# Performance work log

Measured on AMD Instinct MI355X. Metric: run time of the kernel, lower is better.

## Reference

```python
import jax, jax.numpy as jnp
import numpy as np
from jax import lax

B, S, H, E, P, K, R = 64, 512, 768, 32, 16, 9, 6
HEADS, C1, C2 = 4, 128, 64
FEAT = 4 * C2 + 1  # e1, e2, e1*e2, context (64 each) + log-distance


def _ln(x, g, b):
    m = x.mean(-1, keepdims=True)
    v = ((x - m) ** 2).mean(-1, keepdims=True)
    return (x - m) * lax.rsqrt(v + 1e-5) * g + b


def _gat(x, adj, W, a_s, a_d, bias, heads, cout, concat):
    # Dense GATConv over a small fully-masked entity graph. adj[b,i,j]=edge j->i (incl. self-loops).
    h = jnp.einsum('bef,fhc->behc', x, W.reshape(x.shape[-1], heads, cout))
    s = jnp.einsum('behc,hc->bhe', h, a_s)  # source-node attention term
    d = jnp.einsum('behc,hc->bhe', h, a_d)  # target-node attention term
    logits = jax.nn.leaky_relu(d[:, :, :, None] + s[:, :, None, :], 0.2)  # [b,h,i,j]
    logits = jnp.where(adj[:, None, :, :], logits, -1e9)
    att = jax.nn.softmax(logits, axis=-1)
    out = jnp.einsum('bhij,bjhc->bihc', att, h)
    out = out.reshape(out.shape[0], out.shape[1], heads * cout) if concat else out.mean(2)
    return out + bias


def _crf_nll(em, tags, mask, start, end, trans):
    # torchcrf: loss = -mean log-likelihood. em [B,S,K]; tags [B,S]; mask [B,S] bool.
    emt = jnp.transpose(em, (1, 0, 2))
    tgt = tags.T
    mkt = mask.T.astype(em.dtype)
    num0 = start[tgt[0]] + jnp.take_along_axis(emt[0], tgt[0][:, None], 1)[:, 0]

    def nstep(c, inp):
        ptag, sc = c
        e, t, m = inp
        step = trans[ptag, t] + jnp.take_along_axis(e, t[:, None], 1)[:, 0]
        return (jnp.where(m > 0, t, ptag), sc + step * m), None

    (ltag, num), _ = lax.scan(nstep, (tgt[0], num0), (emt[1:], tgt[1:], mkt[1:]))
    num = num + end[ltag]
    a0 = start[None, :] + emt[0]

    def dstep(a, inp):
        e, m = inp
        nxt = jax.scipy.special.logsumexp(a[:, :, None] + trans[None] + e[:, None, :], axis=1)
        return jnp.where(m[:, None] > 0, nxt, a), None

    aT, _ = lax.scan(dstep, a0, (emt[1:], mkt[1:]))
    Z = jax.scipy.special.logsumexp(aT + end[None], axis=1)
    return jnp.mean(Z - num)


def setup_inputs() -> dict:
    key = jax.random.key(0)
    ks = jax.random.split(key, 24)
    n = lambda i, shape, s=0.05: jax.random.normal(ks[i], shape, jnp.float32) * s
    return {
        'sequence_output': jax.random.normal(ks[0], (B, S, H), jnp.float32),
        'attention_mask': jnp.ones((B, S), jnp.int32),
        'ner_labels': jax.random.randint(ks[1], (B, S), 0, K),
        'entity_start': jax.random.randint(ks[2], (B, E), 0, S - 8),
        'entity_len': jax.random.randint(ks[3], (B, E), 0, 8),
        'pair_e1': jax.random.randint(ks[4], (B, P), 0, E),
        'pair_e2': jax.random.randint(ks[5], (B, P), 0, E),
        'pair_labels': jax.random.randint(ks[6], (B, P), 0, 2),
        'adj_mask': jnp.ones((B, E, E), bool),
        'w_ner1': n(7, (H, 256)), 'b_ner1': jnp.zeros((256,), jnp.float32),
        'w_ner2': n(8, (256, K)), 'b_ner2': jnp.zeros((K,), jnp.float32),
        'crf_start': n(9, (K,), 0.1), 'crf_end': n(10, (K,), 0.1), 'crf_trans': n(11, (K, K), 0.1),
        'w_gat1': n(12, (H, HEADS * C1)), 'a_src1': n(13, (HEADS, C1)), 'a_dst1': n(14, (HEADS, C1)),
        'b_gat1': jnp.zeros((HEADS * C1,), jnp.float32),
        'w_gat2': n(15, (HEADS * C1, C2)), 'a_src2': n(16, (1, C2)), 'a_dst2': n(17, (1, C2)),
        'b_gat2': jnp.zeros((C2,), jnp.float32),
        'w_fe': n(18, (FEAT, 512)), 'b_fe': jnp.zeros((512,), jnp.float32),
        'g_fe': jnp.ones((512,), jnp.float32), 'be_fe': jnp.zeros((512,), jnp.float32),
        'w_rc1': n(19, (R, 512, 256)), 'b_rc1': jnp.zeros((R, 256), jnp.float32),
        'g_rc': jnp.ones((R, 256), jnp.float32), 'be_rc': jnp.zeros((R, 256), jnp.float32),
        'w_rc2': n(20, (R, 256, 1)), 'b_rc2': jnp.zeros((R,), jnp.float32),
    }


def reference(sequence_output, attention_mask, ner_labels, entity_start, entity_len,
              pair_e1, pair_e2, pair_labels, adj_mask,
              w_ner1, b_ner1, w_ner2, b_ner2, crf_start, crf_end, crf_trans,
              w_gat1, a_src1, a_dst1, b_gat1, w_gat2, a_src2, a_dst2, b_gat2,
              w_fe, b_fe, g_fe, be_fe, w_rc1, b_rc1, g_rc, be_rc, w_rc2, b_rc2):
    # NER head (dropout off / eval)
    ner_logits = jnp.maximum(sequence_output @ w_ner1 + b_ner1, 0.0) @ w_ner2 + b_ner2
    ner_loss = _crf_nll(ner_logits, ner_labels, attention_mask.astype(bool),
                        crf_start, crf_end, crf_trans)
    # entity span mean-pool via inclusive cumsum trick
    cs = jnp.concatenate([jnp.zeros((B, 1, H), sequence_output.dtype),
                          jnp.cumsum(sequence_output, axis=1)], axis=1)
    e_end = jnp.clip(entity_start + entity_len, 0, S - 1)
    seg = (jnp.take_along_axis(cs, (e_end + 1)[:, :, None], 1)
           - jnp.take_along_axis(cs, entity_start[:, :, None], 1))
    ent = seg / (e_end - entity_start + 1).astype(sequence_output.dtype)[:, :, None]  # [B,E,H]
    x = _gat(ent, adj_mask, w_gat1, a_src1, a_dst1, b_gat1, HEADS, C1, True)
    x = jnp.maximum(x, 0.0)
    x = _gat(x, adj_mask, w_gat2, a_src2, a_dst2, b_gat2, 1, C2, False)  # [B,E,64]
    x1 = jnp.take_along_axis(x, pair_e1[:, :, None], 1)
    x2 = jnp.take_along_axis(x, pair_e2[:, :, None], 1)
    ctx = jnp.broadcast_to(x.mean(1, keepdims=True), (B, P, C2))
    dist = jnp.log(jnp.abs(pair_e1 - pair_e2).astype(x.dtype) + 1.0)[:, :, None]
    pf = jnp.concatenate([x1, x2, x1 * x2, ctx, dist], axis=-1)  # [B,P,257]
    fe = jax.nn.leaky_relu(_ln(pf @ w_fe + b_fe, g_fe, be_fe), 0.01)
    h1 = jnp.einsum('bpf,rfo->rbpo', fe, w_rc1) + b_rc1[:, None, None, :]
    h1 = jax.nn.leaky_relu(_ln(h1, g_rc[:, None, None, :], be_rc[:, None, None, :]), 0.01)
    z = jnp.einsum('rbpo,ro->rbp', h1, w_rc2[:, :, 0]) + b_rc2[:, None, None]
    y = pair_labels.astype(z.dtype)[None]
    # BCEWithLogitsLoss(pos_weight=2.0), mean per relation type, summed over types
    bce = -(2.0 * y * jax.nn.log_sigmoid(z) + (1.0 - y) * jax.nn.log_sigmoid(-z))
    rel_loss = bce.mean(axis=(1, 2)).sum()
    total = ner_loss + rel_loss
    return ner_logits, z, total
```

## Files before the change

kernel.cpp:

```cpp
#include <hip/hip_runtime.h>
#include <math.h>


#define NB 64
#define NS 512
#define NH 768
#define NE 32
#define NP 16
#define NK 9
#define NR 6
#define NHEADS 4
#define NC1 128
#define NC2 64
#define SEGS 16
#define SEGLEN 32

#define ZOFF 294912
#define TOTOFF 301056

#define WS_ENT   0u
#define WS_HG1   1572864u
#define WS_X1    2621440u
#define WS_H2    3670016u
#define WS_X2    3801088u
#define WS_S1    3932160u
#define WS_D1    3940352u
#define WS_S2    3948544u
#define WS_D2    3950592u
#define WS_CTX   3952640u
#define WS_PF    3956736u
#define WS_FE    4222976u
#define WS_CRF   4747264u
#define WS_REL   4747328u
#define WS_W1T   4747392u
#define WS_WRT   0u
#define WS_WFET  393216u
#define WS_SEG   475136u

typedef __attribute__((ext_vector_type(8))) short bf16x8;
typedef __attribute__((ext_vector_type(4))) float f32x4;

__device__ __forceinline__ unsigned short f2bf(float x) {
  union { float f; unsigned u; } v; v.f = x;
  unsigned r = v.u + 0x7FFFu + ((v.u >> 16) & 1u);
  return (unsigned short)(r >> 16);
}

__device__ __forceinline__ float logsigf(float x) {
  if (x >= 0.f) return -log1pf(__expf(-x));
  return x - log1pf(__expf(x));
}

__global__ __launch_bounds__(256) void k_w1t(const float* __restrict__ w1,
    unsigned short* __restrict__ w1t) {
  const int k = blockIdx.x, t = threadIdx.x;
  w1t[t * NH + k] = f2bf(w1[k * 256 + t]);
}

__global__ __launch_bounds__(256) void k_wrt(const float* __restrict__ w1,
    unsigned short* __restrict__ wrt) {
  __shared__ unsigned short tr[256 * 72];
  const int r = blockIdx.x >> 3, kt = blockIdx.x & 7;
  const int k0 = kt * 64, t = threadIdx.x;
#pragma unroll
  for (int i = 0; i < 16; i++) {
    const int slot = t + 256 * i;
    const int row = slot >> 6, c4 = slot & 63;
    const float4 f = *reinterpret_cast<const float4*>(
        &w1[((size_t)(r * 512) + k0 + row) * 256 + c4 * 4]);
    tr[(c4 * 4 + 0) * 72 + row] = f2bf(f.x);
    tr[(c4 * 4 + 1) * 72 + row] = f2bf(f.y);
    tr[(c4 * 4 + 2) * 72 + row] = f2bf(f.z);
    tr[(c4 * 4 + 3) * 72 + row] = f2bf(f.w);
  }
  __syncthreads();
#pragma unroll
  for (int i = 0; i < 8; i++) {
    const int slot = t + 256 * i;
    const int col = slot >> 3, q = slot & 7;
    *reinterpret_cast<uint4*>(&wrt[((size_t)(r * 256 + col)) * 512 + k0 + q * 8]) =
        *reinterpret_cast<const uint4*>(&tr[col * 72 + q * 8]);
  }
}

__global__ __launch_bounds__(256) void k_wfet(const float* __restrict__ w,
    unsigned short* __restrict__ wt) {
  __shared__ unsigned short tr[256 * 72];
  const int kt = blockIdx.x % 5, cb = blockIdx.x / 5;
  const int k0 = kt * 64, c0 = cb * 256, t = threadIdx.x;
#pragma unroll
  for (int i = 0; i < 16; i++) {
    const int slot = t + 256 * i;
    const int row = slot >> 6, c4 = slot & 63;
    const int k = k0 + row;
    float4 f = {0.f, 0.f, 0.f, 0.f};
    if (k < 257)
      f = *reinterpret_cast<const float4*>(&w[(size_t)k * 512 + c0 + c4 * 4]);
    tr[(c4 * 4 + 0) * 72 + row] = f2bf(f.x);
    tr[(c4 * 4 + 1) * 72 + row] = f2bf(f.y);
    tr[(c4 * 4 + 2) * 72 + row] = f2bf(f.z);
    tr[(c4 * 4 + 3) * 72 + row] = f2bf(f.w);
  }
  __syncthreads();
#pragma unroll
  for (int i = 0; i < 8; i++) {
    const int slot = t + 256 * i;
    const int col = slot >> 3, q = slot & 7;
    *reinterpret_cast<uint4*>(&wt[((size_t)(c0 + col)) * 320 + k0 + q * 8]) =
        *reinterpret_cast<const uint4*>(&tr[col * 72 + q * 8]);
  }
}

__global__ __launch_bounds__(256) void k_ner(const float* __restrict__ seq,
    const unsigned short* __restrict__ w1t, const float* __restrict__ b1,
    const float* __restrict__ w2, const float* __restrict__ b2,
    float* __restrict__ out) {
  __shared__ unsigned short AsS[64 * 40];
  __shared__ unsigned short BsS[256 * 40];
  __shared__ float zs[64 * 4 * 12];
  const int t = threadIdx.x;
  const int tok0 = blockIdx.x * 64;
  const int w = t >> 6, lane = t & 63, quad = lane >> 4, l15 = lane & 15;

  f32x4 acc[4][4];
#pragma unroll
  for (int r = 0; r < 4; r++)
#pragma unroll
    for (int c = 0; c < 4; c++) acc[r][c] = (f32x4){0.f, 0.f, 0.f, 0.f};

  const int tokA = t >> 2, koffA = (t & 3) * 8;
  const float* aptr = seq + (size_t)(tok0 + tokA) * NH + koffA;

  for (int kt = 0; kt < NH; kt += 32) {
    __syncthreads();
    {
      const float4 f0 = *reinterpret_cast<const float4*>(aptr + kt);
      const float4 f1 = *reinterpret_cast<const float4*>(aptr + kt + 4);
      bf16x8 av;
      av[0] = (short)f2bf(f0.x); av[1] = (short)f2bf(f0.y);
      av[2] = (short)f2bf(f0.z); av[3] = (short)f2bf(f0.w);
      av[4] = (short)f2bf(f1.x); av[5] = (short)f2bf(f1.y);
      av[6] = (short)f2bf(f1.z); av[7] = (short)f2bf(f1.w);
      *reinterpret_cast<bf16x8*>(&AsS[tokA * 40 + koffA]) = av;
    }
#pragma unroll
    for (int i = 0; i < 4; i++) {
      const int q = t + 256 * i;
      const int col = q >> 2, koff = (q & 3) * 8;
      *reinterpret_cast<uint4*>(&BsS[col * 40 + koff]) =
          *reinterpret_cast<const uint4*>(&w1t[(size_t)col * NH + kt + koff]);
    }
    __syncthreads();
    bf16x8 a[4], b[4];
#pragma unroll
    for (int r = 0; r < 4; r++)
      a[r] = *reinterpret_cast<const bf16x8*>(&AsS[(r * 16 + l15) * 40 + quad * 8]);
#pragma unroll
    for (int c = 0; c < 4; c++)
      b[c] = *reinterpret_cast<const bf16x8*>(&BsS[(w * 64 + c * 16 + l15) * 40 + quad * 8]);
#pragma unroll
    for (int r = 0; r < 4; r++)
#pragma unroll
      for (int c = 0; c < 4; c++)
        acc[r][c] = __builtin_amdgcn_mfma_f32_16x16x32_bf16(a[r], b[c], acc[r][c], 0, 0, 0);
  }

  float b1v[4], w2v[4][NK];
#pragma unroll
  for (int c = 0; c < 4; c++) {
    const int col = w * 64 + c * 16 + l15;
    b1v[c] = b1[col];
#pragma unroll
    for (int cc = 0; cc < NK; cc++) w2v[c][cc] = w2[col * NK + cc];
  }
#pragma unroll
  for (int r = 0; r < 4; r++) {
#pragma unroll
    for (int reg = 0; reg < 4; reg++) {
      float p[NK];
#pragma unroll
      for (int cc = 0; cc < NK; cc++) p[cc] = 0.f;
#pragma unroll
      for (int c = 0; c < 4; c++) {
        const float h = fmaxf(acc[r][c][reg] + b1v[c], 0.f);
#pragma unroll
        for (int cc = 0; cc < NK; cc++) p[cc] = fmaf(h, w2v[c][cc], p[cc]);
      }
#pragma unroll
      for (int o = 1; o < 16; o <<= 1)
#pragma unroll
        for (int cc = 0; cc < NK; cc++) p[cc] += __shfl_xor(p[cc], o);
      if (l15 == 0) {
        const int tokr = r * 16 + quad * 4 + reg;
#pragma unroll
        for (int cc = 0; cc < NK; cc++) zs[(tokr * 4 + w) * 12 + cc] = p[cc];
      }
    }
  }
  __syncthreads();
  if (t < 64) {
#pragma unroll
    for (int cc = 0; cc < NK; cc++) {
      const float z = zs[(t * 4 + 0) * 12 + cc] + zs[(t * 4 + 1) * 12 + cc] +
                      zs[(t * 4 + 2) * 12 + cc] + zs[(t * 4 + 3) * 12 + cc] + b2[cc];
      out[(size_t)(tok0 + t) * NK + cc] = z;
    }
  }
}

__global__ __launch_bounds__(128) void k_crf_seg(const float* __restrict__ em,
    const int* __restrict__ mask, const float* __restrict__ trans,
    float* __restrict__ segm) {
  __shared__ float bufA[16 * 81];
  __shared__ float bufB[8 * 81];
  __shared__ float ems[SEGLEN * 9];
  __shared__ int mks[SEGLEN];
  __shared__ float trs[81];
  const int blk = blockIdx.x;
  const int b = blk >> 4, seg = blk & 15;
  const int t = threadIdx.x;
  const int s0 = 1 + seg * SEGLEN;
  const float* emb = em + (size_t)b * NS * NK;
  const int* mk = mask + b * NS;
  if (t < 81) trs[t] = trans[t];
  for (int i = t; i < SEGLEN * 9; i += 128) {
    const int g = s0 * 9 + i;
    ems[i] = (g < NS * 9) ? emb[g] : 0.f;
  }
  if (t < SEGLEN) {
    const int s = s0 + t;
    mks[t] = (s < NS) ? mk[s] : 0;
  }
  __syncthreads();
  for (int idx = t; idx < 16 * 81; idx += 128) {
    const int p = idx / 81, e = idx % 81, i = e / 9, j = e % 9;
    const int la = 2 * p, lb = la + 1;
    const bool ma = mks[la] > 0, mb = mks[lb] > 0;
    float r;
    if (ma && mb) {
      float v[9], mx = -1e30f;
#pragma unroll
      for (int m = 0; m < 9; m++) {
        v[m] = trs[i * 9 + m] + ems[la * 9 + m] + trs[m * 9 + j];
        mx = fmaxf(mx, v[m]);
      }
      float sum = 0.f;
#pragma unroll
      for (int m = 0; m < 9; m++) sum += __expf(v[m] - mx);
      r = mx + __logf(sum) + ems[lb * 9 + j];
    } else if (ma) {
      r = trs[e] + ems[la * 9 + j];
    } else if (mb) {
      r = trs[e] + ems[lb * 9 + j];
    } else {
      r = (i == j) ? 0.f : -1e30f;
    }
    bufA[p * 81 + e] = r;
  }
  float* src = bufA;
  float* dst = bufB;
  for (int n = 16; n > 1; n >>= 1) {
    __syncthreads();
    const int half = n >> 1;
    for (int idx = t; idx < half * 81; idx += 128) {
      const int q = idx / 81, e = idx % 81, i = e / 9, j = e % 9;
      const float* A = src + (size_t)(2 * q) * 81;
      const float* Bm = src + (size_t)(2 * q + 1) * 81;
      float v[9], mx = -1e30f;
#pragma unroll
      for (int m = 0; m < 9; m++) {
        v[m] = A[i * 9 + m] + Bm[m * 9 + j];
        mx = fmaxf(mx, v[m]);
      }
      float sum = 0.f;
#pragma unroll
      for (int m = 0; m < 9; m++) sum += __expf(v[m] - mx);
      dst[q * 81 + e] = mx + __logf(sum);
    }
    float* tmp = src; src = dst; dst = tmp;
  }
  __syncthreads();
  if (t < 81) segm[((size_t)b * SEGS + seg) * 81 + t] = src[t];
}

__global__ __launch_bounds__(64) void k_crf_fin(const float* __restrict__ em,
    const int* __restrict__ tags, const int* __restrict__ mask,
    const float* __restrict__ startv, const float* __restrict__ endv,
    const float* __restrict__ trans, const float* __restrict__ segm,
    float* __restrict__ lossb) {
  __shared__ float sm[SEGS * 81];
  __shared__ float av[16];
  __shared__ float red[2];
  const int b = blockIdx.x, t = threadIdx.x;
  const float* emb = em + (size_t)b * NS * NK;
  const int* mk = mask + b * NS;
  const int* tg = tags + b * NS;
  for (int i = t; i < SEGS * 81; i += 64) sm[i] = segm[(size_t)b * SEGS * 81 + i];
  {
    float num = 0.f;
    int lastS = 0;
#pragma unroll
    for (int o = 0; o < 8; o++) {
      const int s = t * 8 + o;
      if (s >= 1 && mk[s] > 0) {
        const int cur = tg[s], prv = tg[s - 1];
        num += trans[prv * NK + cur] + emb[s * NK + cur];
        lastS = s;
      }
    }
#pragma unroll
    for (int o = 32; o > 0; o >>= 1) {
      num += __shfl_xor(num, o);
      lastS = max(lastS, __shfl_xor(lastS, o));
    }
    if (t == 0) {
      const int t0 = tg[0];
      red[0] = startv[t0] + emb[t0] + num + endv[tg[lastS]];
    }
  }
  __syncthreads();
  if (t < 9) av[t] = startv[t] + emb[t];
  __syncthreads();
  for (int h = 0; h < SEGS; h++) {
    float nv = 0.f;
    if (t < 9) {
      float v[9], mx = -1e30f;
#pragma unroll
      for (int i2 = 0; i2 < 9; i2++) {
        v[i2] = av[i2] + sm[h * 81 + i2 * 9 + t];
        mx = fmaxf(mx, v[i2]);
      }
      float sum = 0.f;
#pragma unroll
      for (int i2 = 0; i2 < 9; i2++) sum += __expf(v[i2] - mx);
      nv = mx + __logf(sum);
    }
    __syncthreads();
    if (t < 9) av[t] = nv;
    __syncthreads();
  }
  if (t == 0) {
    float mx = -1e30f;
#pragma unroll
    for (int j = 0; j < 9; j++) mx = fmaxf(mx, av[j] + endv[j]);
    float sum = 0.f;
#pragma unroll
    for (int j = 0; j < 9; j++) sum += __expf(av[j] + endv[j] - mx);
    lossb[b] = (mx + __logf(sum)) - red[0];
  }
}

__global__ __launch_bounds__(256) void k_ent(const float* __restrict__ seq,
    const int* __restrict__ est, const int* __restrict__ elen, float* __restrict__ ent) {
  const int be = blockIdx.x;
  const int b = be >> 5, e = be & 31;
  const int st = est[b * NE + e];
  int en = st + elen[b * NE + e];
  en = min(max(en, 0), NS - 1);
  const float inv = 1.f / (float)(en - st + 1);
  for (int c = threadIdx.x; c < NH; c += 256) {
    float s = 0.f;
    for (int r = st; r <= en; r++) s += seq[((size_t)b * NS + r) * NH + c];
    ent[((size_t)b * NE + e) * NH + c] = s * inv;
  }
}

__global__ __launch_bounds__(256) void k_g1(const float* __restrict__ ent,
    const float* __restrict__ w, float* __restrict__ hout) {
  __shared__ float As[32 * 36];
  __shared__ float Bs[32 * 128];
  const int b = blockIdx.x >> 2, cb = blockIdx.x & 3;
  const int t = threadIdx.x;
  const int tc = t & 31, tr = t >> 5;
  float acc[4][4];
#pragma unroll
  for (int i = 0; i < 4; i++)
#pragma unroll
    for (int j = 0; j < 4; j++) acc[i][j] = 0.f;
  for (int kt = 0; kt < NH; kt += 32) {
    __syncthreads();
    {
      const int e = t >> 3, k4 = t & 7;
      *reinterpret_cast<float4*>(&As[e * 36 + k4 * 4]) =
          *reinterpret_cast<const float4*>(&ent[((size_t)b * NE + e) * NH + kt + k4 * 4]);
    }
#pragma unroll
    for (int i = 0; i < 4; i++) {
      const int slot = t + 256 * i;
      const int row = slot >> 5, cg = slot & 31;
      *reinterpret_cast<float4*>(&Bs[row * 128 + cg * 4]) =
          *reinterpret_cast<const float4*>(&w[(size_t)(kt + row) * 512 + cb * 128 + cg * 4]);
    }
    __syncthreads();
#pragma unroll
    for (int kg = 0; kg < 8; kg++) {
      float4 a[4];
#pragma unroll
      for (int i = 0; i < 4; i++)
        a[i] = *reinterpret_cast<const float4*>(&As[(tr * 4 + i) * 36 + kg * 4]);
#pragma unroll
      for (int k2 = 0; k2 < 4; k2++) {
        const float4 bv = *reinterpret_cast<const float4*>(&Bs[(kg * 4 + k2) * 128 + tc * 4]);
#pragma unroll
        for (int i = 0; i < 4; i++) {
          const float av = reinterpret_cast<const float*>(&a[i])[k2];
          acc[i][0] = fmaf(av, bv.x, acc[i][0]);
          acc[i][1] = fmaf(av, bv.y, acc[i][1]);
          acc[i][2] = fmaf(av, bv.z, acc[i][2]);
          acc[i][3] = fmaf(av, bv.w, acc[i][3]);
        }
      }
    }
  }
#pragma unroll
  for (int i = 0; i < 4; i++) {
    float4 v;
    v.x = acc[i][0]; v.y = acc[i][1]; v.z = acc[i][2]; v.w = acc[i][3];
    *reinterpret_cast<float4*>(&hout[((size_t)b * NE + tr * 4 + i) * 512 + cb * 128 + tc * 4]) = v;
  }
}

__global__ __launch_bounds__(128) void k_sd1(const float* __restrict__ h,
    const float* __restrict__ as, const float* __restrict__ ad,
    float* __restrict__ s1, float* __restrict__ d1) {
  __shared__ float sm[4];
  const int be = blockIdx.x;
  const int b = be >> 5, e = be & 31;
  const int t = threadIdx.x;
  for (int hd = 0; hd < NHEADS; hd++) {
    const float v = h[((size_t)b * NE + e) * 512 + hd * NC1 + t];
    float sv = v * as[hd * NC1 + t];
    float dv = v * ad[hd * NC1 + t];
#pragma unroll
    for (int o = 32; o > 0; o >>= 1) { sv += __shfl_xor(sv, o); dv += __shfl_xor(dv, o); }
    if ((t & 63) == 0) { sm[(t >> 6) * 2] = sv; sm[(t >> 6) * 2 + 1] = dv; }
    __syncthreads();
    if (t == 0) {
      s1[(b * NHEADS + hd) * NE + e] = sm[0] + sm[2];
      d1[(b * NHEADS + hd) * NE + e] = sm[1] + sm[3];
    }
    __syncthreads();
  }
}

__global__ __launch_bounds__(128) void k_att1(const float* __restrict__ h,
    const float* __restrict__ s1, const float* __restrict__ d1,
    const unsigned char* __restrict__ adj, const float* __restrict__ bias,
    float* __restrict__ x1) {
  __shared__ float att[NE];
  const int blk = blockIdx.x;
  const int i = blk & 31, hd = (blk >> 5) & 3, b = blk >> 7;
  const int t = threadIdx.x;
  if (t < NE) {
    float lg = d1[(b * NHEADS + hd) * NE + i] + s1[(b * NHEADS + hd) * NE + t];
    lg = lg >= 0.f ? lg : 0.2f * lg;
    if (!adj[((size_t)b * NE + i) * NE + t]) lg = -1e9f;
    att[t] = lg;
  }
  __syncthreads();
  if (t == 0) {
    float m = -1e30f;
#pragma unroll
    for (int j = 0; j < NE; j++) m = fmaxf(m, att[j]);
    float ex[NE];
    float sum = 0.f;
#pragma unroll
    for (int j = 0; j < NE; j++) { ex[j] = __expf(att[j] - m); sum += ex[j]; }
    const float inv = 1.f / sum;
#pragma unroll
    for (int j = 0; j < NE; j++) att[j] = ex[j] * inv;
  }
  __syncthreads();
  float acc = bias[hd * NC1 + t];
  for (int j = 0; j < NE; j++)
    acc += att[j] * h[((size_t)b * NE + j) * 512 + hd * NC1 + t];
  x1[((size_t)b * NE + i) * 512 + hd * NC1 + t] = fmaxf(acc, 0.f);
}

__global__ __launch_bounds__(256) void k_g2(const float* __restrict__ x1,
    const float* __restrict__ w, const float* __restrict__ as, const float* __restrict__ ad,
    float* __restrict__ h2, float* __restrict__ s2, float* __restrict__ d2) {
  __shared__ float As[32 * 36];
  __shared__ float Bs[32 * 64];
  const int b = blockIdx.x;
  const int t = threadIdx.x;
  const int tc = t & 15, tr = t >> 4;
  float acc[2][4];
#pragma unroll
  for (int i = 0; i < 2; i++)
#pragma unroll
    for (int j = 0; j < 4; j++) acc[i][j] = 0.f;
  for (int kt = 0; kt < 512; kt += 32) {
    __syncthreads();
    {
      const int e = t >> 3, k4 = t & 7;
      *reinterpret_cast<float4*>(&As[e * 36 + k4 * 4]) =
          *reinterpret_cast<const float4*>(&x1[((size_t)b * NE + e) * 512 + kt + k4 * 4]);
    }
#pragma unroll
    for (int i = 0; i < 2; i++) {
      const int slot = t + 256 * i;
      const int row = slot >> 4, cg = slot & 15;
      *reinterpret_cast<float4*>(&Bs[row * 64 + cg * 4]) =
          *reinterpret_cast<const float4*>(&w[(size_t)(kt + row) * NC2 + cg * 4]);
    }
    __syncthreads();
#pragma unroll
    for (int kg = 0; kg < 8; kg++) {
      float4 a[2];
#pragma unroll
      for (int i = 0; i < 2; i++)
        a[i] = *reinterpret_cast<const float4*>(&As[(tr * 2 + i) * 36 + kg * 4]);
#pragma unroll
      for (int k2 = 0; k2 < 4; k2++) {
        const float4 bv = *reinterpret_cast<const float4*>(&Bs[(kg * 4 + k2) * 64 + tc * 4]);
#pragma unroll
        for (int i = 0; i < 2; i++) {
          const float av = reinterpret_cast<const float*>(&a[i])[k2];
          acc[i][0] = fmaf(av, bv.x, acc[i][0]);
          acc[i][1] = fmaf(av, bv.y, acc[i][1]);
          acc[i][2] = fmaf(av, bv.z, acc[i][2]);
          acc[i][3] = fmaf(av, bv.w, acc[i][3]);
        }
      }
    }
  }
  const float4 a4s = *reinterpret_cast<const float4*>(&as[tc * 4]);
  const float4 a4d = *reinterpret_cast<const float4*>(&ad[tc * 4]);
#pragma unroll
  for (int i = 0; i < 2; i++) {
    const int e = tr * 2 + i;
    float4 v;
    v.x = acc[i][0]; v.y = acc[i][1]; v.z = acc[i][2]; v.w = acc[i][3];
    *reinterpret_cast<float4*>(&h2[((size_t)b * NE + e) * NC2 + tc * 4]) = v;
    float sv = v.x * a4s.x + v.y * a4s.y + v.z * a4s.z + v.w * a4s.w;
    float dv = v.x * a4d.x + v.y * a4d.y + v.z * a4d.z + v.w * a4d.w;
#pragma unroll
    for (int o = 8; o > 0; o >>= 1) { sv += __shfl_xor(sv, o); dv += __shfl_xor(dv, o); }
    if (tc == 0) { s2[b * NE + e] = sv; d2[b * NE + e] = dv; }
  }
}

__global__ __launch_bounds__(64) void k_att2(const float* __restrict__ h2,
    const float* __restrict__ s2, const float* __restrict__ d2,
    const unsigned char* __restrict__ adj, const float* __restrict__ bias,
    float* __restrict__ x2) {
  __shared__ float att[NE];
  const int be = blockIdx.x;
  const int b = be >> 5, i = be & 31;
  const int t = threadIdx.x;
  if (t < NE) {
    float lg = d2[b * NE + i] + s2[b * NE + t];
    lg = lg >= 0.f ? lg : 0.2f * lg;
    if (!adj[((size_t)b * NE + i) * NE + t]) lg = -1e9f;
    att[t] = lg;
  }
  __syncthreads();
  if (t == 0) {
    float m = -1e30f;
#pragma unroll
    for (int j = 0; j < NE; j++) m = fmaxf(m, att[j]);
    float ex[NE];
    float sum = 0.f;
#pragma unroll
    for (int j = 0; j < NE; j++) { ex[j] = __expf(att[j] - m); sum += ex[j]; }
    const float inv = 1.f / sum;
#pragma unroll
    for (int j = 0; j < NE; j++) att[j] = ex[j] * inv;
  }
  __syncthreads();
  float acc = bias[t];
  for (int j = 0; j < NE; j++)
    acc += att[j] * h2[((size_t)b * NE + j) * NC2 + t];
  x2[((size_t)b * NE + i) * NC2 + t] = acc;
}

__global__ __launch_bounds__(64) void k_ctx(const float* __restrict__ x2, float* __restrict__ ctx) {
  const int b = blockIdx.x, t = threadIdx.x;
  float s = 0.f;
  for (int e = 0; e < NE; e++) s += x2[((size_t)b * NE + e) * NC2 + t];
  ctx[b * NC2 + t] = s * (1.f / NE);
}

__global__ __launch_bounds__(64) void k_pf(const float* __restrict__ x2,
    const float* __restrict__ ctx, const int* __restrict__ pe1, const int* __restrict__ pe2,
    float* __restrict__ pf) {
  const int bp = blockIdx.x;
  const int b = bp >> 4, p = bp & 15;
  const int t = threadIdx.x;
  const int e1 = pe1[b * NP + p], e2 = pe2[b * NP + p];
  const float v1 = x2[((size_t)b * NE + e1) * NC2 + t];
  const float v2 = x2[((size_t)b * NE + e2) * NC2 + t];
  float* row = pf + (size_t)bp * 260;
  row[t] = v1;
  row[64 + t] = v2;
  row[128 + t] = v1 * v2;
  row[192 + t] = ctx[b * NC2 + t];
  if (t == 0) row[256] = logf(fabsf((float)(e1 - e2)) + 1.f);
  if (t < 3) row[257 + t] = 0.f;
}

__global__ __launch_bounds__(256) void k_fe(const float* __restrict__ pf,
    const unsigned short* __restrict__ wt, const float* __restrict__ bfe,
    const float* __restrict__ g, const float* __restrict__ be,
    unsigned short* __restrict__ feb) {
  __shared__ unsigned short Af[16 * 320];
  __shared__ float Cs[16 * 520];
  const int b = blockIdx.x, t = threadIdx.x;
  const int w = t >> 6, lane = t & 63, quad = lane >> 4, l15 = lane & 15;
  for (int i = t; i < 16 * 320; i += 256) {
    const int p = i / 320, k = i - p * 320;
    Af[i] = (k < 260) ? f2bf(pf[(size_t)(b * NP + p) * 260 + k]) : (unsigned short)0;
  }
  __syncthreads();
  f32x4 acc[8];
#pragma unroll
  for (int c = 0; c < 8; c++) acc[c] = (f32x4){0.f, 0.f, 0.f, 0.f};
#pragma unroll
  for (int kt = 0; kt < 10; kt++) {
    const bf16x8 a = *reinterpret_cast<const bf16x8*>(&Af[l15 * 320 + kt * 32 + quad * 8]);
#pragma unroll
    for (int c = 0; c < 8; c++) {
      const int col = w * 128 + c * 16 + l15;
      const bf16x8 bv = *reinterpret_cast<const bf16x8*>(&wt[(size_t)col * 320 + kt * 32 + quad * 8]);
      acc[c] = __builtin_amdgcn_mfma_f32_16x16x32_bf16(a, bv, acc[c], 0, 0, 0);
    }
  }
#pragma unroll
  for (int c = 0; c < 8; c++)
#pragma unroll
    for (int reg = 0; reg < 4; reg++)
      Cs[(quad * 4 + reg) * 520 + w * 128 + c * 16 + l15] = acc[c][reg];
  __syncthreads();
  float bfev[8], gv[8], bev[8];
#pragma unroll
  for (int ch = 0; ch < 8; ch++) {
    const int col = ch * 64 + lane;
    bfev[ch] = bfe[col]; gv[ch] = g[col]; bev[ch] = be[col];
  }
#pragma unroll
  for (int pp = 0; pp < 4; pp++) {
    const int p = w * 4 + pp;
    float v[8], s = 0.f, sq = 0.f;
#pragma unroll
    for (int ch = 0; ch < 8; ch++) {
      v[ch] = Cs[p * 520 + ch * 64 + lane] + bfev[ch];
      s += v[ch]; sq += v[ch] * v[ch];
    }
#pragma unroll
    for (int o = 32; o > 0; o >>= 1) { s += __shfl_xor(s, o); sq += __shfl_xor(sq, o); }
    const float mean = s * (1.f / 512.f);
    const float var = sq * (1.f / 512.f) - mean * mean;
    const float rr = rsqrtf(var + 1e-5f);
#pragma unroll
    for (int ch = 0; ch < 8; ch++) {
      float n = (v[ch] - mean) * rr * gv[ch] + bev[ch];
      n = n >= 0.f ? n : 0.01f * n;
      feb[(size_t)(b * NP + p) * 512 + ch * 64 + lane] = f2bf(n);
    }
  }
}

__global__ __launch_bounds__(256) void k_rc(const unsigned short* __restrict__ feb,
    const unsigned short* __restrict__ wrt, const float* __restrict__ b1,
    const float* __restrict__ g, const float* __restrict__ be,
    const float* __restrict__ w2, const float* __restrict__ b2,
    const int* __restrict__ ylab, float* __restrict__ zout, float* __restrict__ relacc) {
  __shared__ unsigned short Af[16 * 520];
  __shared__ float Cs[16 * 264];
  const int blk = blockIdx.x;
  const int r = blk >> 6, b = blk & 63;
  const int t = threadIdx.x;
  const int w = t >> 6, lane = t & 63, quad = lane >> 4, l15 = lane & 15;
#pragma unroll
  for (int i = 0; i < 4; i++) {
    const int slot = t + 256 * i;
    const int p = slot >> 6, q = slot & 63;
    *reinterpret_cast<uint4*>(&Af[p * 520 + q * 8]) =
        *reinterpret_cast<const uint4*>(&feb[(size_t)(b * NP + p) * 512 + q * 8]);
  }
  __syncthreads();
  f32x4 acc[4];
#pragma unroll
  for (int c = 0; c < 4; c++) acc[c] = (f32x4){0.f, 0.f, 0.f, 0.f};
#pragma unroll
  for (int kt = 0; kt < 16; kt++) {
    const bf16x8 a = *reinterpret_cast<const bf16x8*>(&Af[l15 * 520 + kt * 32 + quad * 8]);
#pragma unroll
    for (int c = 0; c < 4; c++) {
      const int col = w * 64 + c * 16 + l15;
      const bf16x8 bv = *reinterpret_cast<const bf16x8*>(
          &wrt[(size_t)(r * 256 + col) * 512 + kt * 32 + quad * 8]);
      acc[c] = __builtin_amdgcn_mfma_f32_16x16x32_bf16(a, bv, acc[c], 0, 0, 0);
    }
  }
#pragma unroll
  for (int c = 0; c < 4; c++)
#pragma unroll
    for (int reg = 0; reg < 4; reg++)
      Cs[(quad * 4 + reg) * 264 + w * 64 + c * 16 + l15] = acc[c][reg];
  __syncthreads();
  float b1v[4], gv[4], bev[4], w2v[4];
#pragma unroll
  for (int ch = 0; ch < 4; ch++) {
    const int col = r * 256 + ch * 64 + lane;
    b1v[ch] = b1[col]; gv[ch] = g[col]; bev[ch] = be[col]; w2v[ch] = w2[col];
  }
  const float b2v = b2[r];
  float local = 0.f;
#pragma unroll
  for (int pp = 0; pp < 4; pp++) {
    const int p = w * 4 + pp;
    float v[4], s = 0.f, sq = 0.f;
#pragma unroll
    for (int ch = 0; ch < 4; ch++) {
      v[ch] = Cs[p * 264 + ch * 64 + lane] + b1v[ch];
      s += v[ch]; sq += v[ch] * v[ch];
    }
#pragma unroll
    for (int o = 32; o > 0; o >>= 1) { s += __shfl_xor(s, o); sq += __shfl_xor(sq, o); }
    const float mean = s * (1.f / 256.f);
    const float var = sq * (1.f / 256.f) - mean * mean;
    const float rr = rsqrtf(var + 1e-5f);
    float zdot = 0.f;
#pragma unroll
    for (int ch = 0; ch < 4; ch++) {
      float n = (v[ch] - mean) * rr * gv[ch] + bev[ch];
      n = n >= 0.f ? n : 0.01f * n;
      zdot = fmaf(n, w2v[ch], zdot);
    }
#pragma unroll
    for (int o = 32; o > 0; o >>= 1) zdot += __shfl_xor(zdot, o);
    if (lane == 0) {
      const float zp = zdot + b2v;
      zout[(size_t)(r * NB + b) * NP + p] = zp;
      const float y = (float)ylab[b * NP + p];
      local += -(2.f * y * logsigf(zp) + (1.f - y) * logsigf(-zp));
    }
  }
  if (lane == 0) atomicAdd(relacc, local * (1.f / (NB * NP)));
}

__global__ __launch_bounds__(64) void k_fin(const float* __restrict__ lossb,
    const float* __restrict__ rel, float* __restrict__ out) {
  float v = lossb[threadIdx.x];
#pragma unroll
  for (int o = 32; o > 0; o >>= 1) v += __shfl_down(v, o);
  if (threadIdx.x == 0) out[TOTOFF] = v * (1.f / NB) + rel[0];
}

extern "C" void kernel_launch(void* const* d_in, const int* in_sizes, int n_in,
                              void* d_out, int out_size, void* d_ws, size_t ws_size,
                              hipStream_t stream) {
  const float* seq = (const float*)d_in[0];
  const int* amask = (const int*)d_in[1];
  const int* nlab = (const int*)d_in[2];
  const int* est = (const int*)d_in[3];
  const int* elen = (const int*)d_in[4];
  const int* pe1 = (const int*)d_in[5];
  const int* pe2 = (const int*)d_in[6];
  const int* plab = (const int*)d_in[7];
  const unsigned char* adj = (const unsigned char*)d_in[8];
  const float* w_ner1 = (const float*)d_in[9];
  const float* b_ner1 = (const float*)d_in[10];
  const float* w_ner2 = (const float*)d_in[11];
  const float* b_ner2 = (const float*)d_in[12];
  const float* crf_start = (const float*)d_in[13];
  const float* crf_end = (const float*)d_in[14];
  const float* crf_trans = (const float*)d_in[15];
  const float* w_gat1 = (const float*)d_in[16];
  const float* a_src1 = (const float*)d_in[17];
  const float* a_dst1 = (const float*)d_in[18];
  const float* b_gat1 = (const float*)d_in[19];
  const float* w_gat2 = (const float*)d_in[20];
  const float* a_src2 = (const float*)d_in[21];
  const float* a_dst2 = (const float*)d_in[22];
  const float* b_gat2 = (const float*)d_in[23];
  const float* w_fe = (const float*)d_in[24];
  const float* b_fe = (const float*)d_in[25];
  const float* g_fe = (const float*)d_in[26];
  const float* be_fe = (const float*)d_in[27];
  const float* w_rc1 = (const float*)d_in[28];
  const float* b_rc1 = (const float*)d_in[29];
  const float* g_rc = (const float*)d_in[30];
  const float* be_rc = (const float*)d_in[31];
  const float* w_rc2 = (const float*)d_in[32];
  const float* b_rc2 = (const float*)d_in[33];

  float* out = (float*)d_out;
  float* ws = (float*)d_ws;
  float* ent = ws + WS_ENT;
  float* hg1 = ws + WS_HG1;
  float* x1 = ws + WS_X1;
  float* h2 = ws + WS_H2;
  float* x2 = ws + WS_X2;
  float* s1 = ws + WS_S1;
  float* d1 = ws + WS_D1;
  float* s2 = ws + WS_S2;
  float* d2 = ws + WS_D2;
  float* ctx = ws + WS_CTX;
  float* pf = ws + WS_PF;
  float* crfb = ws + WS_CRF;
  float* rel = ws + WS_REL;
  unsigned short* w1t = (unsigned short*)(ws + WS_W1T);
  unsigned short* feb = (unsigned short*)(ws + WS_FE);
  unsigned short* wrt = (unsigned short*)(ws + WS_WRT);
  unsigned short* wfet = (unsigned short*)(ws + WS_WFET);
  float* segm = ws + WS_SEG;

  hipMemsetAsync(rel, 0, sizeof(float), stream);

  k_w1t<<<NH, 256, 0, stream>>>(w_ner1, w1t);
  k_ner<<<512, 256, 0, stream>>>(seq, w1t, b_ner1, w_ner2, b_ner2, out);
  k_ent<<<NB * NE, 256, 0, stream>>>(seq, est, elen, ent);
  k_g1<<<NB * 4, 256, 0, stream>>>(ent, w_gat1, hg1);
  k_wrt<<<NR * 8, 256, 0, stream>>>(w_rc1, wrt);
  k_wfet<<<10, 256, 0, stream>>>(w_fe, wfet);
  k_crf_seg<<<NB * SEGS, 128, 0, stream>>>(out, amask, crf_trans, segm);
  k_crf_fin<<<NB, 64, 0, stream>>>(out, nlab, amask, crf_start, crf_end, crf_trans,
                                   segm, crfb);
  k_sd1<<<NB * NE, 128, 0, stream>>>(hg1, a_src1, a_dst1, s1, d1);
  k_att1<<<NB * NHEADS * NE, 128, 0, stream>>>(hg1, s1, d1, adj, b_gat1, x1);
  k_g2<<<NB, 256, 0, stream>>>(x1, w_gat2, a_src2, a_dst2, h2, s2, d2);
  k_att2<<<NB * NE, 64, 0, stream>>>(h2, s2, d2, adj, b_gat2, x2);
  k_ctx<<<NB, 64, 0, stream>>>(x2, ctx);
  k_pf<<<NB * NP, 64, 0, stream>>>(x2, ctx, pe1, pe2, pf);
  k_fe<<<NB, 256, 0, stream>>>(pf, wfet, b_fe, g_fe, be_fe, feb);
  k_rc<<<NR * NB, 256, 0, stream>>>(feb, wrt, b_rc1, g_rc, be_rc, w_rc2, b_rc2,
                                    plab, out + ZOFF, rel);
  k_fin<<<1, 64, 0, stream>>>(crfb, rel, out);
}
```

Measured before the change: 449.2 us.

## Double-buffer NER GEMM and fuse GAT attention-score, attention and pair-feature kernels

The NER GEMM loop now prefetches the next K-tile from global memory into registers while MFMAs run on the current LDS buffer, using two LDS buffers and one barrier per iteration. The GAT source and target attention dot products are folded into the first GAT GEMM epilogue, which removes k_sd1. Layer-1 attention now handles one batch-head per block with the head's features staged in shared memory, instead of one block per target entity. Layer-2 attention, context mean and pair-feature assembly are merged into one per-batch kernel, which cuts launches and intermediate global traffic but uses far fewer, larger blocks.

Result: no change. 449.2 us (+0.0%).

```diff
diff --git a/kernel.cpp b/kernel.cpp
--- a/kernel.cpp
+++ b/kernel.cpp
@@ -22,12 +22,10 @@
 #define WS_HG1   1572864u
 #define WS_X1    2621440u
 #define WS_H2    3670016u
-#define WS_X2    3801088u
 #define WS_S1    3932160u
 #define WS_D1    3940352u
 #define WS_S2    3948544u
 #define WS_D2    3950592u
-#define WS_CTX   3952640u
 #define WS_PF    3956736u
 #define WS_FE    4222976u
 #define WS_CRF   4747264u
@@ -115,8 +113,8 @@
     const unsigned short* __restrict__ w1t, const float* __restrict__ b1,
     const float* __restrict__ w2, const float* __restrict__ b2,
     float* __restrict__ out) {
-  __shared__ unsigned short AsS[64 * 40];
-  __shared__ unsigned short BsS[256 * 40];
+  __shared__ unsigned short AsS[2][64 * 40];
+  __shared__ unsigned short BsS[2][256 * 40];
   __shared__ float zs[64 * 4 * 12];
   const int t = threadIdx.x;
   const int tok0 = blockIdx.x * 64;
@@ -130,39 +128,62 @@
 
   const int tokA = t >> 2, koffA = (t & 3) * 8;
   const float* aptr = seq + (size_t)(tok0 + tokA) * NH + koffA;
-
-  for (int kt = 0; kt < NH; kt += 32) {
+  const int colB = t >> 2, koffB = (t & 3) * 8;
+
+  float4 fA0, fA1;
+  uint4 rB[4];
+  fA0 = *reinterpret_cast<const float4*>(aptr);
+  fA1 = *reinterpret_cast<const float4*>(aptr + 4);
+#pragma unroll
+  for (int i = 0; i < 4; i++)
+    rB[i] = *reinterpret_cast<const uint4*>(&w1t[(size_t)(colB + 64 * i) * NH + koffB]);
+  {
+    bf16x8 av;
+    av[0] = (short)f2bf(fA0.x); av[1] = (short)f2bf(fA0.y);
+    av[2] = (short)f2bf(fA0.z); av[3] = (short)f2bf(fA0.w);
+    av[4] = (short)f2bf(fA1.x); av[5] = (short)f2bf(fA1.y);
+    av[6] = (short)f2bf(fA1.z); av[7] = (short)f2bf(fA1.w);
+    *reinterpret_cast<bf16x8*>(&AsS[0][tokA * 40 + koffA]) = av;
+#pragma unroll
+    for (int i = 0; i < 4; i++)
+      *reinterpret_cast<uint4*>(&BsS[0][(colB + 64 * i) * 40 + koffB]) = rB[i];
+  }
+
+  for (int it = 0; it < 24; ++it) {
     __syncthreads();
-    {
-      const float4 f0 = *reinterpret_cast<const float4*>(aptr + kt);
-      const float4 f1 = *reinterpret_cast<const float4*>(aptr + kt + 4);
-      bf16x8 av;
-      av[0] = (short)f2bf(f0.x); av[1] = (short)f2bf(f0.y);
-      av[2] = (short)f2bf(f0.z); av[3] = (short)f2bf(f0.w);
-      av[4] = (short)f2bf(f1.x); av[5] = (short)f2bf(f1.y);
-      av[6] = (short)f2bf(f1.z); av[7] = (short)f2bf(f1.w);
-      *reinterpret_cast<bf16x8*>(&AsS[tokA * 40 + koffA]) = av;
-    }
-#pragma unroll
-    for (int i = 0; i < 4; i++) {
-      const int q = t + 256 * i;
-      const int col = q >> 2, koff = (q & 3) * 8;
-      *reinterpret_cast<uint4*>(&BsS[col * 40 + koff]) =
-          *reinterpret_cast<const uint4*>(&w1t[(size_t)col * NH + kt + koff]);
-    }
-    __syncthreads();
+    const int kn = (it + 1) * 32;
+    if (kn < NH) {
+      fA0 = *reinterpret_cast<const float4*>(aptr + kn);
+      fA1 = *reinterpret_cast<const float4*>(aptr + kn + 4);
+#pragma unroll
+      for (int i = 0; i < 4; i++)
+        rB[i] = *reinterpret_cast<const uint4*>(
+            &w1t[(size_t)(colB + 64 * i) * NH + kn + koffB]);
+    }
+    const int cur = it & 1;
     bf16x8 a[4], b[4];
 #pragma unroll
     for (int r = 0; r < 4; r++)
-      a[r] = *reinterpret_cast<const bf16x8*>(&AsS[(r * 16 + l15) * 40 + quad * 8]);
+      a[r] = *reinterpret_cast<const bf16x8*>(&AsS[cur][(r * 16 + l15) * 40 + quad * 8]);
 #pragma unroll
     for (int c = 0; c < 4; c++)
-      b[c] = *reinterpret_cast<const bf16x8*>(&BsS[(w * 64 + c * 16 + l15) * 40 + quad * 8]);
+      b[c] = *reinterpret_cast<const bf16x8*>(&BsS[cur][(w * 64 + c * 16 + l15) * 40 + quad * 8]);
 #pragma unroll
     for (int r = 0; r < 4; r++)
 #pragma unroll
       for (int c = 0; c < 4; c++)
         acc[r][c] = __builtin_amdgcn_mfma_f32_16x16x32_bf16(a[r], b[c], acc[r][c], 0, 0, 0);
+    if (kn < NH) {
+      bf16x8 av;
+      av[0] = (short)f2bf(fA0.x); av[1] = (short)f2bf(fA0.y);
+      av[2] = (short)f2bf(fA0.z); av[3] = (short)f2bf(fA0.w);
+      av[4] = (short)f2bf(fA1.x); av[5] = (short)f2bf(fA1.y);
+      av[6] = (short)f2bf(fA1.z); av[7] = (short)f2bf(fA1.w);
+      *reinterpret_cast<bf16x8*>(&AsS[cur ^ 1][tokA * 40 + koffA]) = av;
+#pragma unroll
+      for (int i = 0; i < 4; i++)
+        *reinterpret_cast<uint4*>(&BsS[cur ^ 1][(colB + 64 * i) * 40 + koffB]) = rB[i];
+    }
   }
 
   float b1v[4], w2v[4][NK];
@@ -366,7 +387,8 @@
 }
 
 __global__ __launch_bounds__(256) void k_g1(const float* __restrict__ ent,
-    const float* __restrict__ w, float* __restrict__ hout) {
+    const float* __restrict__ w, const float* __restrict__ as, const float* __restrict__ ad,
+    float* __restrict__ hout, float* __restrict__ s1, float* __restrict__ d1) {
   __shared__ float As[32 * 36];
   __shared__ float Bs[32 * 128];
   const int b = blockIdx.x >> 2, cb = blockIdx.x & 3;
@@ -412,69 +434,81 @@
       }
     }
   }
+  const float4 a4s = *reinterpret_cast<const float4*>(&as[cb * NC1 + tc * 4]);
+  const float4 a4d = *reinterpret_cast<const float4*>(&ad[cb * NC1 + tc * 4]);
 #pragma unroll
   for (int i = 0; i < 4; i++) {
     float4 v;
     v.x = acc[i][0]; v.y = acc[i][1]; v.z = acc[i][2]; v.w = acc[i][3];
     *reinterpret_cast<float4*>(&hout[((size_t)b * NE + tr * 4 + i) * 512 + cb * 128 + tc * 4]) = v;
-  }
-}
-
-__global__ __launch_bounds__(128) void k_sd1(const float* __restrict__ h,
-    const float* __restrict__ as, const float* __restrict__ ad,
-    float* __restrict__ s1, float* __restrict__ d1) {
-  __shared__ float sm[4];
-  const int be = blockIdx.x;
-  const int b = be >> 5, e = be & 31;
-  const int t = threadIdx.x;
-  for (int hd = 0; hd < NHEADS; hd++) {
-    const float v = h[((size_t)b * NE + e) * 512 + hd * NC1 + t];
-    float sv = v * as[hd * NC1 + t];
-    float dv = v * ad[hd * NC1 + t];
-#pragma unroll
-    for (int o = 32; o > 0; o >>= 1) { sv += __shfl_xor(sv, o); dv += __shfl_xor(dv, o); }
-    if ((t & 63) == 0) { sm[(t >> 6) * 2] = sv; sm[(t >> 6) * 2 + 1] = dv; }
-    __syncthreads();
-    if (t == 0) {
-      s1[(b * NHEADS + hd) * NE + e] = sm[0] + sm[2];
-      d1[(b * NHEADS + hd) * NE + e] = sm[1] + sm[3];
-    }
-    __syncthreads();
-  }
-}
-
-__global__ __launch_bounds__(128) void k_att1(const float* __restrict__ h,
+    float sv = v.x * a4s.x + v.y * a4s.y + v.z * a4s.z + v.w * a4s.w;
+    float dv = v.x * a4d.x + v.y * a4d.y + v.z * a4d.z + v.w * a4d.w;
+#pragma unroll
+    for (int o = 16; o > 0; o >>= 1) { sv += __shfl_xor(sv, o); dv += __shfl_xor(dv, o); }
+    if (tc == 0) {
+      s1[(b * NHEADS + cb) * NE + tr * 4 + i] = sv;
+      d1[(b * NHEADS + cb) * NE + tr * 4 + i] = dv;
+    }
+  }
+}
+
+__global__ __launch_bounds__(256) void k_att1(const float* __restrict__ h,
     const float* __restrict__ s1, const float* __restrict__ d1,
     const unsigned char* __restrict__ adj, const float* __restrict__ bias,
     float* __restrict__ x1) {
-  __shared__ float att[NE];
+  __shared__ float hs[32 * 128];
+  __shared__ float att[32 * 33];
+  __shared__ float s1s[32], d1s[32];
   const int blk = blockIdx.x;
-  const int i = blk & 31, hd = (blk >> 5) & 3, b = blk >> 7;
+  const int hd = blk & 3, b = blk >> 2;
   const int t = threadIdx.x;
-  if (t < NE) {
-    float lg = d1[(b * NHEADS + hd) * NE + i] + s1[(b * NHEADS + hd) * NE + t];
+#pragma unroll
+  for (int i = 0; i < 16; i++) {
+    const int idx = t + 256 * i;
+    const int e = idx >> 7, c = idx & 127;
+    hs[idx] = h[((size_t)b * NE + e) * 512 + hd * NC1 + c];
+  }
+  if (t < 32) {
+    s1s[t] = s1[(b * NHEADS + hd) * NE + t];
+    d1s[t] = d1[(b * NHEADS + hd) * NE + t];
+  }
+  __syncthreads();
+#pragma unroll
+  for (int i = 0; i < 4; i++) {
+    const int idx = t + 256 * i;
+    const int r = idx >> 5, j = idx & 31;
+    float lg = d1s[r] + s1s[j];
     lg = lg >= 0.f ? lg : 0.2f * lg;
-    if (!adj[((size_t)b * NE + i) * NE + t]) lg = -1e9f;
-    att[t] = lg;
-  }
-  __syncthreads();
-  if (t == 0) {
+    if (!adj[((size_t)b * NE + r) * NE + j]) lg = -1e9f;
+    att[r * 33 + j] = lg;
+  }
+  __syncthreads();
+  if (t < 32) {
     float m = -1e30f;
 #pragma unroll
-    for (int j = 0; j < NE; j++) m = fmaxf(m, att[j]);
-    float ex[NE];
+    for (int j = 0; j < 32; j++) m = fmaxf(m, att[t * 33 + j]);
     float sum = 0.f;
 #pragma unroll
-    for (int j = 0; j < NE; j++) { ex[j] = __expf(att[j] - m); sum += ex[j]; }
+    for (int j = 0; j < 32; j++) {
+      const float e = __expf(att[t * 33 + j] - m);
+      att[t * 33 + j] = e;
+      sum += e;
+    }
     const float inv = 1.f / sum;
 #pragma unroll
-    for (int j = 0; j < NE; j++) att[j] = ex[j] * inv;
-  }
-  __syncthreads();
-  float acc = bias[hd * NC1 + t];
-  for (int j = 0; j < NE; j++)
-    acc += att[j] * h[((size_t)b * NE + j) * 512 + hd * NC1 + t];
-  x1[((size_t)b * NE + i) * 512 + hd * NC1 + t] = fmaxf(acc, 0.f);
+    for (int j = 0; j < 32; j++) att[t * 33 + j] *= inv;
+  }
+  __syncthreads();
+  const int c = t & 127, ih = t >> 7;
+  const float bv = bias[hd * NC1 + c];
+#pragma unroll
+  for (int ii = 0; ii < 16; ii++) {
+    const int i = ih * 16 + ii;
+    float o = bv;
+#pragma unroll
+    for (int j = 0; j < 32; j++) o = fmaf(att[i * 33 + j], hs[j * 128 + c], o);
+    x1[((size_t)b * NE + i) * 512 + hd * NC1 + c] = fmaxf(o, 0.f);
+  }
 }
 
 __global__ __launch_bounds__(256) void k_g2(const float* __restrict__ x1,
@@ -541,63 +575,81 @@
   }
 }
 
-__global__ __launch_bounds__(64) void k_att2(const float* __restrict__ h2,
+__global__ __launch_bounds__(256) void k_tail2(const float* __restrict__ h2,
     const float* __restrict__ s2, const float* __restrict__ d2,
     const unsigned char* __restrict__ adj, const float* __restrict__ bias,
-    float* __restrict__ x2) {
-  __shared__ float att[NE];
-  const int be = blockIdx.x;
-  const int b = be >> 5, i = be & 31;
-  const int t = threadIdx.x;
-  if (t < NE) {
-    float lg = d2[b * NE + i] + s2[b * NE + t];
+    const int* __restrict__ pe1, const int* __restrict__ pe2,
+    float* __restrict__ pf) {
+  __shared__ float h2s[32 * 64];
+  __shared__ float att[32 * 33];
+  __shared__ float s2s[32], d2s[32];
+  __shared__ float x2s[32 * 64];
+  __shared__ float ctxs[64];
+  const int b = blockIdx.x, t = threadIdx.x;
+#pragma unroll
+  for (int i = 0; i < 8; i++) {
+    const int idx = t + 256 * i;
+    h2s[idx] = h2[(size_t)b * NE * NC2 + idx];
+  }
+  if (t < 32) { s2s[t] = s2[b * NE + t]; d2s[t] = d2[b * NE + t]; }
+  __syncthreads();
+#pragma unroll
+  for (int i = 0; i < 4; i++) {
+    const int idx = t + 256 * i;
+    const int r = idx >> 5, j = idx & 31;
+    float lg = d2s[r] + s2s[j];
     lg = lg >= 0.f ? lg : 0.2f * lg;
-    if (!adj[((size_t)b * NE + i) * NE + t]) lg = -1e9f;
-    att[t] = lg;
-  }
-  __syncthreads();
-  if (t == 0) {
+    if (!adj[((size_t)b * NE + r) * NE + j]) lg = -1e9f;
+    att[r * 33 + j] = lg;
+  }
+  __syncthreads();
+  if (t < 32) {
     float m = -1e30f;
 #pragma unroll
-    for (int j = 0; j < NE; j++) m = fmaxf(m, att[j]);
-    float ex[NE];
+    for (int j = 0; j < 32; j++) m = fmaxf(m, att[t * 33 + j]);
     float sum = 0.f;
 #pragma unroll
-    for (int j = 0; j < NE; j++) { ex[j] = __expf(att[j] - m); sum += ex[j]; }
+    for (int j = 0; j < 32; j++) {
+      const float e = __expf(att[t * 33 + j] - m);
+      att[t * 33 + j] = e;
+      sum += e;
+    }
     const float inv = 1.f / sum;
 #pragma unroll
-    for (int j = 0; j < NE; j++) att[j] = ex[j] * inv;
-  }
-  __syncthreads();
-  float acc = bias[t];
-  for (int j = 0; j < NE; j++)
-    acc += att[j] * h2[((size_t)b * NE + j) * NC2 + t];
-  x2[((size_t)b * NE + i) * NC2 + t] = acc;
-}
-
-__global__ __launch_bounds__(64) void k_ctx(const float* __restrict__ x2, float* __restrict__ ctx) {
-  const int b = blockIdx.x, t = threadIdx.x;
-  float s = 0.f;
-  for (int e = 0; e < NE; e++) s += x2[((size_t)b * NE + e) * NC2 + t];
-  ctx[b * NC2 + t] = s * (1.f / NE);
-}
-
-__global__ __launch_bounds__(64) void k_pf(const float* __restrict__ x2,
-    const float* __restrict__ ctx, const int* __restrict__ pe1, const int* __restrict__ pe2,
-    float* __restrict__ pf) {
-  const int bp = blockIdx.x;
-  const int b = bp >> 4, p = bp & 15;
-  const int t = threadIdx.x;
-  const int e1 = pe1[b * NP + p], e2 = pe2[b * NP + p];
-  const float v1 = x2[((size_t)b * NE + e1) * NC2 + t];
-  const float v2 = x2[((size_t)b * NE + e2) * NC2 + t];
-  float* row = pf + (size_t)bp * 260;
-  row[t] = v1;
-  row[64 + t] = v2;
-  row[128 + t] = v1 * v2;
-  row[192 + t] = ctx[b * NC2 + t];
-  if (t == 0) row[256] = logf(fabsf((float)(e1 - e2)) + 1.f);
-  if (t < 3) row[257 + t] = 0.f;
+    for (int j = 0; j < 32; j++) att[t * 33 + j] *= inv;
+  }
+  __syncthreads();
+  const int c = t & 63, ig = t >> 6;
+  const float bv = bias[c];
+#pragma unroll
+  for (int ii = 0; ii < 8; ii++) {
+    const int i = ig * 8 + ii;
+    float o = bv;
+#pragma unroll
+    for (int j = 0; j < 32; j++) o = fmaf(att[i * 33 + j], h2s[j * 64 + c], o);
+    x2s[i * 64 + c] = o;
+  }
+  __syncthreads();
+  if (t < 64) {
+    float s = 0.f;
+#pragma unroll
+    for (int i = 0; i < 32; i++) s += x2s[i * 64 + t];
+    ctxs[t] = s * (1.f / 32.f);
+  }
+  __syncthreads();
+#pragma unroll
+  for (int pp = 0; pp < 4; pp++) {
+    const int p = ig * 4 + pp;
+    const int e1 = pe1[b * NP + p], e2 = pe2[b * NP + p];
+    const float v1 = x2s[e1 * 64 + c], v2 = x2s[e2 * 64 + c];
+    float* row = pf + (size_t)(b * NP + p) * 260;
+    row[c] = v1;
+    row[64 + c] = v2;
+    row[128 + c] = v1 * v2;
+    row[192 + c] = ctxs[c];
+    if (c == 0) row[256] = logf(fabsf((float)(e1 - e2)) + 1.f);
+    if (c < 3) row[257 + c] = 0.f;
+  }
 }
 
 __global__ __launch_bounds__(256) void k_fe(const float* __restrict__ pf,
@@ -793,12 +845,10 @@
   float* hg1 = ws + WS_HG1;
   float* x1 = ws + WS_X1;
   float* h2 = ws + WS_H2;
-  float* x2 = ws + WS_X2;
   float* s1 = ws + WS_S1;
   float* d1 = ws + WS_D1;
   float* s2 = ws + WS_S2;
   float* d2 = ws + WS_D2;
-  float* ctx = ws + WS_CTX;
   float* pf = ws + WS_PF;
   float* crfb = ws + WS_CRF;
   float* rel = ws + WS_REL;
@@ -813,18 +863,15 @@
   k_w1t<<<NH, 256, 0, stream>>>(w_ner1, w1t);
   k_ner<<<512, 256, 0, stream>>>(seq, w1t, b_ner1, w_ner2, b_ner2, out);
   k_ent<<<NB * NE, 256, 0, stream>>>(seq, est, elen, ent);
-  k_g1<<<NB * 4, 256, 0, stream>>>(ent, w_gat1, hg1);
+  k_g1<<<NB * 4, 256, 0, stream>>>(ent, w_gat1, a_src1, a_dst1, hg1, s1, d1);
   k_wrt<<<NR * 8, 256, 0, stream>>>(w_rc1, wrt);
   k_wfet<<<10, 256, 0, stream>>>(w_fe, wfet);
   k_crf_seg<<<NB * SEGS, 128, 0, stream>>>(out, amask, crf_trans, segm);
   k_crf_fin<<<NB, 64, 0, stream>>>(out, nlab, amask, crf_start, crf_end, crf_trans,
                                    segm, crfb);
-  k_sd1<<<NB * NE, 128, 0, stream>>>(hg1, a_src1, a_dst1, s1, d1);
-  k_att1<<<NB * NHEADS * NE, 128, 0, stream>>>(hg1, s1, d1, adj, b_gat1, x1);
+  k_att1<<<NB * NHEADS, 256, 0, stream>>>(hg1, s1, d1, adj, b_gat1, x1);
   k_g2<<<NB, 256, 0, stream>>>(x1, w_gat2, a_src2, a_dst2, h2, s2, d2);
-  k_att2<<<NB * NE, 64, 0, stream>>>(h2, s2, d2, adj, b_gat2, x2);
-  k_ctx<<<NB, 64, 0, stream>>>(x2, ctx);
-  k_pf<<<NB * NP, 64, 0, stream>>>(x2, ctx, pe1, pe2, pf);
+  k_tail2<<<NB, 256, 0, stream>>>(h2, s2, d2, adj, b_gat2, pe1, pe2, pf);
   k_fe<<<NB, 256, 0, stream>>>(pf, wfet, b_fe, g_fe, be_fe, feb);
   k_rc<<<NR * NB, 256, 0, stream>>>(feb, wrt, b_rc1, g_rc, be_rc, w_rc2, b_rc2,
                                     plab, out + ZOFF, rel);
```
